# Kernel optimization log

Measured on AMD Instinct MI355X. Metric: run time of the kernel, lower is better.

The kernel has to match this reference:

```python
import jax, jax.numpy as jnp
import numpy as np
import math

D_MODEL = 512
D_HEAD = 64
N_HEADS = D_MODEL // D_HEAD  # 8
COND = 768
K = 7        # neighborhood kernel size
EPS = 1e-6


def _rope_freqs():
    # RoPE(dim=d_head//2, n_heads): freqs geometric in [pi, 10*pi), shape [n_heads, d_head//4]
    dim = D_HEAD // 2
    n = N_HEADS * dim // 2
    freqs = jnp.exp(jnp.linspace(math.log(math.pi), math.log(10.0 * math.pi), n + 1)[:-1])
    return freqs.reshape(dim // 2, N_HEADS).T  # [nh, d_head//4]


def _rms_norm(x, scale, eps):
    mean_sq = jnp.mean(x * x, axis=-1, keepdims=True)
    return x * (scale * jax.lax.rsqrt(mean_sq + eps))


def _apply_rotary(x, theta):
    # rotate first 2*d dims of head dim, leave the rest untouched
    d = theta.shape[-1]
    x1, x2, rest = x[..., :d], x[..., d:2 * d], x[..., 2 * d:]
    cos, sin = jnp.cos(theta), jnp.sin(theta)
    return jnp.concatenate([x1 * cos - x2 * sin, x2 * cos + x1 * sin, rest], axis=-1)


def _nb_idx(L, k):
    # NATTEN border handling: window shifts (clamps) so every query sees exactly k keys
    i = np.arange(L)
    start = np.clip(i - k // 2, 0, L - k)
    return jnp.asarray(start[:, None] + np.arange(k)[None, :])  # [L, k]


def setup_inputs() -> dict:
    key = jax.random.key(0)
    ks = jax.random.split(key, 7)
    N, H, W = 2, 32, 32
    x = jax.random.normal(ks[0], (N, H, W, D_MODEL), jnp.float32)
    pos = jax.random.uniform(ks[1], (N, H, W, 1), jnp.float32, -1.0, 1.0)
    cond = jax.random.normal(ks[2], (N, COND), jnp.float32)
    w_cond = jax.random.normal(ks[3], (D_MODEL, COND), jnp.float32) * 0.02
    w_qkv = jax.random.normal(ks[4], (3 * D_MODEL, D_MODEL), jnp.float32) * 0.02
    scale = jnp.full((N_HEADS,), 10.0, jnp.float32)
    w_out = jax.random.normal(ks[5], (D_MODEL, D_MODEL), jnp.float32) * 0.02
    return {"x": x, "pos": pos, "cond": cond, "w_cond": w_cond,
            "w_qkv": w_qkv, "scale": scale, "w_out": w_out}


def reference(x, pos, cond, w_cond, w_qkv, scale, w_out):
    N, H, W, C = x.shape
    skip = x
    # AdaRMSNorm: rms_norm(x, linear(cond) + 1)
    norm_scale = cond @ w_cond.T + 1.0                  # [N, C]
    xn = _rms_norm(x, norm_scale[:, None, None, :], EPS)
    # qkv projection -> [3, N, nh, H, W, e]
    qkv = (xn @ w_qkv.T).reshape(N, H, W, 3, N_HEADS, D_HEAD)
    qkv = qkv.transpose(3, 0, 4, 1, 2, 5)
    q, k, v = qkv[0], qkv[1], qkv[2]                    # [N, nh, H, W, e]
    # cosine-sim scaling
    sq = jnp.sqrt(scale)[:, None, None, None]           # [nh,1,1,1]
    q = q * (sq * jax.lax.rsqrt(jnp.sum(q * q, -1, keepdims=True) + 1e-6))
    k = k * (sq * jax.lax.rsqrt(jnp.sum(k * k, -1, keepdims=True) + 1e-6))
    # RoPE
    theta = pos[..., None, :] * _rope_freqs()           # [N,H,W,nh,e/4]
    theta = jnp.moveaxis(theta, -2, -4)                 # [N,nh,H,W,e/4]
    q = _apply_rotary(q, theta)
    k = _apply_rotary(k, theta)
    # 2D neighborhood attention (NATTEN, dilation 1)
    ih, iw = _nb_idx(H, K), _nb_idx(W, K)
    Knb = k[:, :, ih][:, :, :, :, iw]                   # [N,nh,H,K,W,K,e]
    Vnb = v[:, :, ih][:, :, :, :, iw]
    qk = jnp.einsum('ncije,nciajbe->ncijab', q, Knb)    # [N,nh,H,W,K,K]
    a = jax.nn.softmax(qk.reshape(N, N_HEADS, H, W, K * K), axis=-1)
    a = a.reshape(N, N_HEADS, H, W, K, K)
    o = jnp.einsum('ncijab,nciajbe->ncije', a, Vnb)     # [N,nh,H,W,e]
    o = o.transpose(0, 2, 3, 1, 4).reshape(N, H, W, C)
    return o @ w_out.T + skip
```

## Files before the change

kernel.cpp:

```cpp
#include <hip/hip_runtime.h>

typedef unsigned short u16;
typedef unsigned int u32;
typedef __bf16 bf16x8 __attribute__((ext_vector_type(8)));
typedef float f32x4 __attribute__((ext_vector_type(4)));

__device__ __forceinline__ float bf2f(u16 v) {
    union { u32 u; float f; } c; c.u = ((u32)v) << 16; return c.f;
}
__device__ __forceinline__ u16 f2bf(float f) {
    union { float f; u32 u; } c; c.f = f;
    u32 u = c.u + 0x7fffu + ((c.u >> 16) & 1u);
    return (u16)(u >> 16);
}

__global__ __launch_bounds__(256) void cond_kernel(
    const float* __restrict__ cond, const float* __restrict__ w_cond, float* __restrict__ ns)
{
    int lane = threadIdx.x & 63;
    int wid = blockIdx.x * 4 + (threadIdx.x >> 6);
    int n = wid >> 9, c = wid & 511;
    const float* cp = cond + n * 768;
    const float* wp = w_cond + (size_t)c * 768;
    float s = 0.f;
    #pragma unroll
    for (int j = 0; j < 12; j++)
        s += cp[lane + j * 64] * wp[lane + j * 64];
    #pragma unroll
    for (int d = 1; d < 64; d <<= 1) s += __shfl_xor(s, d);
    if (lane == 0) ns[wid] = s + 1.f;
}

__global__ __launch_bounds__(256) void prep_kernel(
    const float* __restrict__ x, const float* __restrict__ ns,
    const float* __restrict__ w_qkv, const float* __restrict__ w_out,
    u16* __restrict__ xn, u16* __restrict__ wqkvb, u16* __restrict__ woutb)
{
    int b = blockIdx.x;
    if (b < 512) {
        int w = threadIdx.x >> 6, lane = threadIdx.x & 63;
        int p = b * 4 + w;
        int n = p >> 10;
        const float* xp = x + (size_t)p * 512;
        const float* nsp = ns + n * 512;
        float4 v0 = *(const float4*)(xp + lane * 4);
        float4 v1 = *(const float4*)(xp + 256 + lane * 4);
        float ss = v0.x * v0.x + v0.y * v0.y + v0.z * v0.z + v0.w * v0.w
                 + v1.x * v1.x + v1.y * v1.y + v1.z * v1.z + v1.w * v1.w;
        #pragma unroll
        for (int d = 1; d < 64; d <<= 1) ss += __shfl_xor(ss, d);
        float inv = rsqrtf(ss * (1.f / 512.f) + 1e-6f);
        float4 n0 = *(const float4*)(nsp + lane * 4);
        float4 n1 = *(const float4*)(nsp + 256 + lane * 4);
        ushort4 o0, o1;
        o0.x = f2bf(v0.x * n0.x * inv); o0.y = f2bf(v0.y * n0.y * inv);
        o0.z = f2bf(v0.z * n0.z * inv); o0.w = f2bf(v0.w * n0.w * inv);
        o1.x = f2bf(v1.x * n1.x * inv); o1.y = f2bf(v1.y * n1.y * inv);
        o1.z = f2bf(v1.z * n1.z * inv); o1.w = f2bf(v1.w * n1.w * inv);
        *(ushort4*)(xn + (size_t)p * 512 + lane * 4) = o0;
        *(ushort4*)(xn + (size_t)p * 512 + 256 + lane * 4) = o1;
    } else {
        const float* src; u16* dst; size_t i4;
        if (b < 1280) { src = w_qkv; dst = wqkvb; i4 = (size_t)(b - 512)  * 1024 + threadIdx.x * 4; }
        else          { src = w_out; dst = woutb; i4 = (size_t)(b - 1280) * 1024 + threadIdx.x * 4; }
        float4 v = *(const float4*)(src + i4);
        ushort4 o; o.x = f2bf(v.x); o.y = f2bf(v.y); o.z = f2bf(v.z); o.w = f2bf(v.w);
        *(ushort4*)(dst + i4) = o;
    }
}

__global__ __launch_bounds__(256) void gemm_qkv(
    const u16* __restrict__ A, const u16* __restrict__ B,
    const float* __restrict__ pos, const float* __restrict__ scale,
    u16* __restrict__ qp, u16* __restrict__ kp, u16* __restrict__ vp)
{
    __shared__ __align__(16) u16 As[4][64][40];
    __shared__ __align__(16) u16 Bs[4][64][40];
    int tid = threadIdx.x;
    int lane = tid & 63;
    int w = tid >> 6;
    int wm = w >> 1, wn = w & 1;
    int bm = blockIdx.x * 64, bn = blockIdx.y * 64;
    int qk = blockIdx.y >> 3, h = blockIdx.y & 7;
    int lrow = tid >> 2, lc8 = (tid & 3) * 8;

    f32x4 zero = {0.f, 0.f, 0.f, 0.f};
    f32x4 acc[2][2];
    acc[0][0] = zero; acc[0][1] = zero; acc[1][0] = zero; acc[1][1] = zero;

    const u16* Ap = A + (size_t)(bm + lrow) * 512 + lc8;
    const u16* Bp = B + (size_t)(bn + lrow) * 512 + lc8;
    int m = lane & 15, quad = lane >> 4, kq = quad * 8;

    for (int k0 = 0; k0 < 512; k0 += 128) {
        #pragma unroll
        for (int s = 0; s < 4; s++) {
            *(uint4*)&As[s][lrow][lc8] = *(const uint4*)(Ap + k0 + s * 32);
            *(uint4*)&Bs[s][lrow][lc8] = *(const uint4*)(Bp + k0 + s * 32);
        }
        __syncthreads();
        #pragma unroll
        for (int kk = 0; kk < 4; kk++)
        #pragma unroll
        for (int ri = 0; ri < 2; ri++) {
            bf16x8 af = *(const bf16x8*)&As[kk][wm * 32 + ri * 16 + m][kq];
            #pragma unroll
            for (int ci = 0; ci < 2; ci++) {
                bf16x8 bfr = *(const bf16x8*)&Bs[kk][wn * 32 + ci * 16 + m][kq];
                acc[ri][ci] = __builtin_amdgcn_mfma_f32_16x16x32_bf16(af, bfr, acc[ri][ci], 0, 0, 0);
            }
        }
        __syncthreads();
    }

    float invn[2][4];
    if (qk < 2) {
        float* red = (float*)As;
        #pragma unroll
        for (int ri = 0; ri < 2; ri++)
        #pragma unroll
        for (int reg = 0; reg < 4; reg++) {
            float pa = acc[ri][0][reg] * acc[ri][0][reg]
                     + acc[ri][1][reg] * acc[ri][1][reg];
            #pragma unroll
            for (int d = 1; d < 16; d <<= 1) pa += __shfl_xor(pa, d);
            if (m == 0) red[(wm * 32 + ri * 16 + quad * 4 + reg) * 2 + wn] = pa;
        }
        __syncthreads();
        float sq = sqrtf(scale[h]);
        #pragma unroll
        for (int ri = 0; ri < 2; ri++)
        #pragma unroll
        for (int reg = 0; reg < 4; reg++) {
            int rl = wm * 32 + ri * 16 + quad * 4 + reg;
            invn[ri][reg] = sq * rsqrtf(red[rl * 2] + red[rl * 2 + 1] + 1e-6f);
        }
    }
    u16* plane = (qk == 0) ? qp : (qk == 1) ? kp : vp;
    float fr = 3.14159265358979323846f * expf((float)(m * 8 + h) * (2.302585092994046f / 128.f));
    #pragma unroll
    for (int ri = 0; ri < 2; ri++)
    #pragma unroll
    for (int reg = 0; reg < 4; reg++) {
        int rl = wm * 32 + ri * 16 + quad * 4 + reg;
        int p = bm + rl;
        size_t basep = ((size_t)((p >> 10) * 8 + h) * 1024 + (p & 1023)) * 64;
        float v0 = acc[ri][0][reg], v1 = acc[ri][1][reg];
        if (qk < 2) {
            float ivn = invn[ri][reg];
            v0 *= ivn; v1 *= ivn;
            if (wn == 0) {
                float th = pos[p] * fr;
                float cs = cosf(th), sn = sinf(th);
                float o0 = v0 * cs - v1 * sn;
                float o1 = v1 * cs + v0 * sn;
                v0 = o0; v1 = o1;
            }
        }
        plane[basep + wn * 32 + m]      = f2bf(v0);
        plane[basep + wn * 32 + 16 + m] = f2bf(v1);
    }
}

__global__ __launch_bounds__(256) void gemm_out(
    const u16* __restrict__ A, const u16* __restrict__ B,
    float* __restrict__ C, const float* __restrict__ skip, int N, int K)
{
    __shared__ __align__(16) u16 As[4][64][40];
    __shared__ __align__(16) u16 Bs[4][64][40];
    int tid = threadIdx.x;
    int lane = tid & 63;
    int w = tid >> 6;
    int wm = w >> 1, wn = w & 1;
    int bm = blockIdx.x * 64, bn = blockIdx.y * 64;
    int lrow = tid >> 2, lc8 = (tid & 3) * 8;

    f32x4 zero = {0.f, 0.f, 0.f, 0.f};
    f32x4 acc[2][2];
    acc[0][0] = zero; acc[0][1] = zero; acc[1][0] = zero; acc[1][1] = zero;

    const u16* Ap = A + (size_t)(bm + lrow) * K + lc8;
    const u16* Bp = B + (size_t)(bn + lrow) * K + lc8;
    int r = lane & 15, kq = (lane >> 4) * 8;

    for (int k0 = 0; k0 < K; k0 += 128) {
        #pragma unroll
        for (int s = 0; s < 4; s++) {
            *(uint4*)&As[s][lrow][lc8] = *(const uint4*)(Ap + k0 + s * 32);
            *(uint4*)&Bs[s][lrow][lc8] = *(const uint4*)(Bp + k0 + s * 32);
        }
        __syncthreads();
        #pragma unroll
        for (int kk = 0; kk < 4; kk++)
        #pragma unroll
        for (int ri = 0; ri < 2; ri++) {
            bf16x8 af = *(const bf16x8*)&As[kk][wm * 32 + ri * 16 + r][kq];
            #pragma unroll
            for (int ci = 0; ci < 2; ci++) {
                bf16x8 bfr = *(const bf16x8*)&Bs[kk][wn * 32 + ci * 16 + r][kq];
                acc[ri][ci] = __builtin_amdgcn_mfma_f32_16x16x32_bf16(af, bfr, acc[ri][ci], 0, 0, 0);
            }
        }
        __syncthreads();
    }

    #pragma unroll
    for (int ri = 0; ri < 2; ri++)
    #pragma unroll
    for (int ci = 0; ci < 2; ci++) {
        int col = bn + wn * 32 + ci * 16 + (lane & 15);
        int row0 = bm + wm * 32 + ri * 16 + (lane >> 4) * 4;
        #pragma unroll
        for (int reg = 0; reg < 4; reg++) {
            size_t idx = (size_t)(row0 + reg) * N + col;
            C[idx] = acc[ri][ci][reg] + skip[idx];
        }
    }
}

__global__ __launch_bounds__(256) void attn_mfma(
    const u16* __restrict__ qp, const u16* __restrict__ kp, const u16* __restrict__ vp,
    u16* __restrict__ ob)
{
    __shared__ __align__(16) u16 Kb[208 * 72];
    __shared__ __align__(16) u16 Sb[64 * 232];

    int tid = threadIdx.x, lane = tid & 63, w = tid >> 6;
    int bx = blockIdx.x;
    int n = bx >> 7, h = (bx >> 4) & 7, t = bx & 15;
    int ti = (t >> 2) * 8, tj = (t & 3) * 8;
    int r0 = min(max(ti - 3, 0), 18), c0 = min(max(tj - 3, 0), 18);
    const u16* qpl = qp + ((size_t)(n * 8 + h) << 16);
    const u16* kpl = kp + ((size_t)(n * 8 + h) << 16);
    const u16* vpl = vp + ((size_t)(n * 8 + h) << 16);

    for (int g = tid; g < 1568; g += 256) {
        int nb = g >> 3, k8 = (g & 7) << 3;
        int ar = nb / 14, ac = nb - ar * 14;
        *(uint4*)&Kb[nb * 72 + k8] =
            *(const uint4*)&kpl[(size_t)((r0 + ar) * 32 + c0 + ac) * 64 + k8];
    }
    __syncthreads();

    int m = lane & 15, quad = lane >> 4;
    {
        int r = w * 16 + m;
        int tok = (ti + (r >> 3)) * 32 + (tj + (r & 7));
        bf16x8 qf0 = *(const bf16x8*)&qpl[(size_t)tok * 64 + quad * 8];
        bf16x8 qf1 = *(const bf16x8*)&qpl[(size_t)tok * 64 + 32 + quad * 8];
        _Float16* sp = (_Float16*)Sb;
        #pragma unroll
        for (int nt = 0; nt < 13; nt++) {
            f32x4 acc = {0.f, 0.f, 0.f, 0.f};
            bf16x8 b0 = *(const bf16x8*)&Kb[(nt * 16 + m) * 72 + quad * 8];
            bf16x8 b1 = *(const bf16x8*)&Kb[(nt * 16 + m) * 72 + 32 + quad * 8];
            acc = __builtin_amdgcn_mfma_f32_16x16x32_bf16(qf0, b0, acc, 0, 0, 0);
            acc = __builtin_amdgcn_mfma_f32_16x16x32_bf16(qf1, b1, acc, 0, 0, 0);
            #pragma unroll
            for (int reg = 0; reg < 4; reg++)
                sp[(w * 16 + quad * 4 + reg) * 232 + nt * 16 + m] = (_Float16)acc[reg];
        }
    }
    __syncthreads();

    for (int g = tid; g < 1568; g += 256) {
        int nb = g >> 3, k8 = (g & 7) << 3;
        int ar = nb / 14, ac = nb - ar * 14;
        uint4 v4 = *(const uint4*)&vpl[(size_t)((r0 + ar) * 32 + c0 + ac) * 64 + k8];
        u32 uu[4] = {v4.x, v4.y, v4.z, v4.w};
        #pragma unroll
        for (int e = 0; e < 4; e++) {
            Kb[(k8 + 2 * e) * 234 + nb]     = (u16)(uu[e] & 0xffff);
            Kb[(k8 + 2 * e + 1) * 234 + nb] = (u16)(uu[e] >> 16);
        }
    }
    for (int g = tid; g < 1792; g += 256) {
        int d = g / 28, nb = 196 + (g - d * 28);
        Kb[d * 234 + nb] = 0;
    }

    {
        int l16 = lane & 15, g4 = lane >> 4;
        #pragma unroll
        for (int it = 0; it < 4; it++) {
            int rr = w * 16 + it * 4 + g4;
            int i2 = ti + (rr >> 3), j2 = tj + (rr & 7);
            int alo = min(max(i2 - 3, 0), 25) - r0;
            int blo = min(max(j2 - 3, 0), 25) - c0;
            const _Float16* sp = (const _Float16*)&Sb[rr * 232];
            float vals[14];
            float mx = -1e30f;
            #pragma unroll
            for (int c = 0; c < 14; c++) {
                int col = l16 + c * 16;
                float v = -1e30f;
                if (col < 196) {
                    int ar = col / 14, ac = col - ar * 14;
                    if (ar >= alo && ar < alo + 7 && ac >= blo && ac < blo + 7)
                        v = (float)sp[col];
                }
                vals[c] = v; mx = fmaxf(mx, v);
            }
            #pragma unroll
            for (int d = 1; d < 16; d <<= 1) mx = fmaxf(mx, __shfl_xor(mx, d));
            float s = 0.f;
            #pragma unroll
            for (int c = 0; c < 14; c++) {
                float e = (vals[c] > -1e29f) ? expf(vals[c] - mx) : 0.f;
                vals[c] = e; s += e;
            }
            #pragma unroll
            for (int d = 1; d < 16; d <<= 1) s += __shfl_xor(s, d);
            float rs = __frcp_rn(s);
            u16* pp = &Sb[rr * 232];
            #pragma unroll
            for (int c = 0; c < 14; c++)
                pp[l16 + c * 16] = f2bf(vals[c] * rs);
        }
    }
    __syncthreads();

    f32x4 oacc[4];
    #pragma unroll
    for (int nt = 0; nt < 4; nt++) { f32x4 z = {0.f,0.f,0.f,0.f}; oacc[nt] = z; }
    #pragma unroll
    for (int ks = 0; ks < 7; ks++) {
        bf16x8 pa = *(const bf16x8*)&Sb[(w * 16 + m) * 232 + ks * 32 + quad * 8];
        #pragma unroll
        for (int nt = 0; nt < 4; nt++) {
            int ad = (nt * 16 + m) * 234 + ks * 32 + quad * 8;
            union { u32 u[4]; bf16x8 v; } vb;
            vb.u[0] = *(const u32*)&Kb[ad];
            vb.u[1] = *(const u32*)&Kb[ad + 2];
            vb.u[2] = *(const u32*)&Kb[ad + 4];
            vb.u[3] = *(const u32*)&Kb[ad + 6];
            oacc[nt] = __builtin_amdgcn_mfma_f32_16x16x32_bf16(pa, vb.v, oacc[nt], 0, 0, 0);
        }
    }
    #pragma unroll
    for (int nt = 0; nt < 4; nt++) {
        #pragma unroll
        for (int reg = 0; reg < 4; reg++) {
            int rr = w * 16 + quad * 4 + reg;
            int tok = (ti + (rr >> 3)) * 32 + (tj + (rr & 7));
            ob[(size_t)(n * 1024 + tok) * 512 + h * 64 + nt * 16 + m] = f2bf(oacc[nt][reg]);
        }
    }
}

extern "C" void kernel_launch(void* const* d_in, const int* in_sizes, int n_in,
                              void* d_out, int out_size, void* d_ws, size_t ws_size,
                              hipStream_t stream)
{
    const float *x = nullptr, *pos = nullptr, *cond = nullptr, *w_cond = nullptr,
                *w_qkv = nullptr, *scale = nullptr, *w_out = nullptr;
    for (int i = 0; i < n_in; i++) {
        switch (in_sizes[i]) {
            case 1048576: x      = (const float*)d_in[i]; break;
            case 2048:    pos    = (const float*)d_in[i]; break;
            case 1536:    cond   = (const float*)d_in[i]; break;
            case 393216:  w_cond = (const float*)d_in[i]; break;
            case 786432:  w_qkv  = (const float*)d_in[i]; break;
            case 8:       scale  = (const float*)d_in[i]; break;
            case 262144:  w_out  = (const float*)d_in[i]; break;
            default: break;
        }
    }
    float* out = (float*)d_out;

    char* ws = (char*)d_ws;
    float* ns    = (float*)ws;
    u16*   wqkvb = (u16*)(ws + 12288);
    u16*   woutb = (u16*)(ws + 12288 + 1572864);
    u16*   xn    = (u16*)(ws + 12288 + 2097152);
    u16*   qp    = (u16*)(ws + 12288 + 4194304);
    u16*   kp    = (u16*)(ws + 12288 + 6291456);
    u16*   vp    = (u16*)(ws + 12288 + 8388608);
    u16*   ob    = (u16*)(ws + 12288 + 10485760);

    cond_kernel<<<256, 256, 0, stream>>>(cond, w_cond, ns);
    prep_kernel<<<1536, 256, 0, stream>>>(x, ns, w_qkv, w_out, xn, wqkvb, woutb);
    gemm_qkv<<<dim3(32, 24), 256, 0, stream>>>(xn, wqkvb, pos, scale, qp, kp, vp);
    attn_mfma<<<256, 256, 0, stream>>>(qp, kp, vp, ob);
    gemm_out<<<dim3(32, 8), 256, 0, stream>>>(ob, woutb, out, x, 512, 512);
}
```

Before: 109.9 us.

## Rebalance prep kernels, double attention block threads, hoist MFMA fragment loads

Moves the weight bf16 conversion into the cond kernel and gives RMS-norm its own launch, so the cond matvec and the weight casts share one grid. The attention kernel now runs 512 threads per block: QK tiles, softmax rows and PV output columns are split across 8 waves, and s_setprio is raised around the MFMAs. The exp mask check is replaced with exp2f. Both GEMM inner loops load their A/B fragments once per k-step before issuing four MFMAs. More waves per attention block mean more parallelism over the same LDS buffers, but also more barrier cost and an uneven 7/6 split of the 13 QK tiles.

```diff
diff --git a/kernel.cpp b/kernel.cpp
--- a/kernel.cpp
+++ b/kernel.cpp
@@ -14,59 +14,60 @@
     return (u16)(u >> 16);
 }
 
-__global__ __launch_bounds__(256) void cond_kernel(
-    const float* __restrict__ cond, const float* __restrict__ w_cond, float* __restrict__ ns)
-{
-    int lane = threadIdx.x & 63;
-    int wid = blockIdx.x * 4 + (threadIdx.x >> 6);
-    int n = wid >> 9, c = wid & 511;
-    const float* cp = cond + n * 768;
-    const float* wp = w_cond + (size_t)c * 768;
-    float s = 0.f;
-    #pragma unroll
-    for (int j = 0; j < 12; j++)
-        s += cp[lane + j * 64] * wp[lane + j * 64];
-    #pragma unroll
-    for (int d = 1; d < 64; d <<= 1) s += __shfl_xor(s, d);
-    if (lane == 0) ns[wid] = s + 1.f;
-}
-
-__global__ __launch_bounds__(256) void prep_kernel(
-    const float* __restrict__ x, const float* __restrict__ ns,
+__global__ __launch_bounds__(256) void cond_prepw_kernel(
+    const float* __restrict__ cond, const float* __restrict__ w_cond, float* __restrict__ ns,
     const float* __restrict__ w_qkv, const float* __restrict__ w_out,
-    u16* __restrict__ xn, u16* __restrict__ wqkvb, u16* __restrict__ woutb)
+    u16* __restrict__ wqkvb, u16* __restrict__ woutb)
 {
     int b = blockIdx.x;
-    if (b < 512) {
-        int w = threadIdx.x >> 6, lane = threadIdx.x & 63;
-        int p = b * 4 + w;
-        int n = p >> 10;
-        const float* xp = x + (size_t)p * 512;
-        const float* nsp = ns + n * 512;
-        float4 v0 = *(const float4*)(xp + lane * 4);
-        float4 v1 = *(const float4*)(xp + 256 + lane * 4);
-        float ss = v0.x * v0.x + v0.y * v0.y + v0.z * v0.z + v0.w * v0.w
-                 + v1.x * v1.x + v1.y * v1.y + v1.z * v1.z + v1.w * v1.w;
-        #pragma unroll
-        for (int d = 1; d < 64; d <<= 1) ss += __shfl_xor(ss, d);
-        float inv = rsqrtf(ss * (1.f / 512.f) + 1e-6f);
-        float4 n0 = *(const float4*)(nsp + lane * 4);
-        float4 n1 = *(const float4*)(nsp + 256 + lane * 4);
-        ushort4 o0, o1;
-        o0.x = f2bf(v0.x * n0.x * inv); o0.y = f2bf(v0.y * n0.y * inv);
-        o0.z = f2bf(v0.z * n0.z * inv); o0.w = f2bf(v0.w * n0.w * inv);
-        o1.x = f2bf(v1.x * n1.x * inv); o1.y = f2bf(v1.y * n1.y * inv);
-        o1.z = f2bf(v1.z * n1.z * inv); o1.w = f2bf(v1.w * n1.w * inv);
-        *(ushort4*)(xn + (size_t)p * 512 + lane * 4) = o0;
-        *(ushort4*)(xn + (size_t)p * 512 + 256 + lane * 4) = o1;
+    if (b < 256) {
+        int lane = threadIdx.x & 63;
+        int wid = b * 4 + (threadIdx.x >> 6);
+        int n = wid >> 9, c = wid & 511;
+        const float* cp = cond + n * 768;
+        const float* wp = w_cond + (size_t)c * 768;
+        float s = 0.f;
+        #pragma unroll
+        for (int j = 0; j < 12; j++)
+            s += cp[lane + j * 64] * wp[lane + j * 64];
+        #pragma unroll
+        for (int d = 1; d < 64; d <<= 1) s += __shfl_xor(s, d);
+        if (lane == 0) ns[wid] = s + 1.f;
     } else {
         const float* src; u16* dst; size_t i4;
-        if (b < 1280) { src = w_qkv; dst = wqkvb; i4 = (size_t)(b - 512)  * 1024 + threadIdx.x * 4; }
-        else          { src = w_out; dst = woutb; i4 = (size_t)(b - 1280) * 1024 + threadIdx.x * 4; }
+        if (b < 1024) { src = w_qkv; dst = wqkvb; i4 = (size_t)(b - 256)  * 1024 + threadIdx.x * 4; }
+        else          { src = w_out; dst = woutb; i4 = (size_t)(b - 1024) * 1024 + threadIdx.x * 4; }
         float4 v = *(const float4*)(src + i4);
         ushort4 o; o.x = f2bf(v.x); o.y = f2bf(v.y); o.z = f2bf(v.z); o.w = f2bf(v.w);
         *(ushort4*)(dst + i4) = o;
     }
+}
+
+__global__ __launch_bounds__(256) void rms_kernel(
+    const float* __restrict__ x, const float* __restrict__ ns, u16* __restrict__ xn)
+{
+    int b = blockIdx.x;
+    int w = threadIdx.x >> 6, lane = threadIdx.x & 63;
+    int p = b * 4 + w;
+    int n = p >> 10;
+    const float* xp = x + (size_t)p * 512;
+    const float* nsp = ns + n * 512;
+    float4 v0 = *(const float4*)(xp + lane * 4);
+    float4 v1 = *(const float4*)(xp + 256 + lane * 4);
+    float ss = v0.x * v0.x + v0.y * v0.y + v0.z * v0.z + v0.w * v0.w
+             + v1.x * v1.x + v1.y * v1.y + v1.z * v1.z + v1.w * v1.w;
+    #pragma unroll
+    for (int d = 1; d < 64; d <<= 1) ss += __shfl_xor(ss, d);
+    float inv = rsqrtf(ss * (1.f / 512.f) + 1e-6f);
+    float4 n0 = *(const float4*)(nsp + lane * 4);
+    float4 n1 = *(const float4*)(nsp + 256 + lane * 4);
+    ushort4 o0, o1;
+    o0.x = f2bf(v0.x * n0.x * inv); o0.y = f2bf(v0.y * n0.y * inv);
+    o0.z = f2bf(v0.z * n0.z * inv); o0.w = f2bf(v0.w * n0.w * inv);
+    o1.x = f2bf(v1.x * n1.x * inv); o1.y = f2bf(v1.y * n1.y * inv);
+    o1.z = f2bf(v1.z * n1.z * inv); o1.w = f2bf(v1.w * n1.w * inv);
+    *(ushort4*)(xn + (size_t)p * 512 + lane * 4) = o0;
+    *(ushort4*)(xn + (size_t)p * 512 + 256 + lane * 4) = o1;
 }
 
 __global__ __launch_bounds__(256) void gemm_qkv(
@@ -100,15 +101,15 @@
         }
         __syncthreads();
         #pragma unroll
-        for (int kk = 0; kk < 4; kk++)
-        #pragma unroll
-        for (int ri = 0; ri < 2; ri++) {
-            bf16x8 af = *(const bf16x8*)&As[kk][wm * 32 + ri * 16 + m][kq];
-            #pragma unroll
-            for (int ci = 0; ci < 2; ci++) {
-                bf16x8 bfr = *(const bf16x8*)&Bs[kk][wn * 32 + ci * 16 + m][kq];
-                acc[ri][ci] = __builtin_amdgcn_mfma_f32_16x16x32_bf16(af, bfr, acc[ri][ci], 0, 0, 0);
-            }
+        for (int kk = 0; kk < 4; kk++) {
+            bf16x8 a0 = *(const bf16x8*)&As[kk][wm * 32 + m][kq];
+            bf16x8 a1 = *(const bf16x8*)&As[kk][wm * 32 + 16 + m][kq];
+            bf16x8 b0 = *(const bf16x8*)&Bs[kk][wn * 32 + m][kq];
+            bf16x8 b1 = *(const bf16x8*)&Bs[kk][wn * 32 + 16 + m][kq];
+            acc[0][0] = __builtin_amdgcn_mfma_f32_16x16x32_bf16(a0, b0, acc[0][0], 0, 0, 0);
+            acc[0][1] = __builtin_amdgcn_mfma_f32_16x16x32_bf16(a0, b1, acc[0][1], 0, 0, 0);
+            acc[1][0] = __builtin_amdgcn_mfma_f32_16x16x32_bf16(a1, b0, acc[1][0], 0, 0, 0);
+            acc[1][1] = __builtin_amdgcn_mfma_f32_16x16x32_bf16(a1, b1, acc[1][1], 0, 0, 0);
         }
         __syncthreads();
     }
@@ -191,15 +192,15 @@
         }
         __syncthreads();
         #pragma unroll
-        for (int kk = 0; kk < 4; kk++)
-        #pragma unroll
-        for (int ri = 0; ri < 2; ri++) {
-            bf16x8 af = *(const bf16x8*)&As[kk][wm * 32 + ri * 16 + r][kq];
-            #pragma unroll
-            for (int ci = 0; ci < 2; ci++) {
-                bf16x8 bfr = *(const bf16x8*)&Bs[kk][wn * 32 + ci * 16 + r][kq];
-                acc[ri][ci] = __builtin_amdgcn_mfma_f32_16x16x32_bf16(af, bfr, acc[ri][ci], 0, 0, 0);
-            }
+        for (int kk = 0; kk < 4; kk++) {
+            bf16x8 a0 = *(const bf16x8*)&As[kk][wm * 32 + r][kq];
+            bf16x8 a1 = *(const bf16x8*)&As[kk][wm * 32 + 16 + r][kq];
+            bf16x8 b0 = *(const bf16x8*)&Bs[kk][wn * 32 + r][kq];
+            bf16x8 b1 = *(const bf16x8*)&Bs[kk][wn * 32 + 16 + r][kq];
+            acc[0][0] = __builtin_amdgcn_mfma_f32_16x16x32_bf16(a0, b0, acc[0][0], 0, 0, 0);
+            acc[0][1] = __builtin_amdgcn_mfma_f32_16x16x32_bf16(a0, b1, acc[0][1], 0, 0, 0);
+            acc[1][0] = __builtin_amdgcn_mfma_f32_16x16x32_bf16(a1, b0, acc[1][0], 0, 0, 0);
+            acc[1][1] = __builtin_amdgcn_mfma_f32_16x16x32_bf16(a1, b1, acc[1][1], 0, 0, 0);
         }
         __syncthreads();
     }
@@ -218,7 +219,7 @@
     }
 }
 
-__global__ __launch_bounds__(256) void attn_mfma(
+__global__ __launch_bounds__(512) void attn_mfma(
     const u16* __restrict__ qp, const u16* __restrict__ kp, const u16* __restrict__ vp,
     u16* __restrict__ ob)
 {
@@ -234,7 +235,7 @@
     const u16* kpl = kp + ((size_t)(n * 8 + h) << 16);
     const u16* vpl = vp + ((size_t)(n * 8 + h) << 16);
 
-    for (int g = tid; g < 1568; g += 256) {
+    for (int g = tid; g < 1568; g += 512) {
         int nb = g >> 3, k8 = (g & 7) << 3;
         int ar = nb / 14, ac = nb - ar * 14;
         *(uint4*)&Kb[nb * 72 + k8] =
@@ -243,27 +244,32 @@
     __syncthreads();
 
     int m = lane & 15, quad = lane >> 4;
+    int rg = w & 3, half = w >> 2;
     {
-        int r = w * 16 + m;
+        int r = rg * 16 + m;
         int tok = (ti + (r >> 3)) * 32 + (tj + (r & 7));
         bf16x8 qf0 = *(const bf16x8*)&qpl[(size_t)tok * 64 + quad * 8];
         bf16x8 qf1 = *(const bf16x8*)&qpl[(size_t)tok * 64 + 32 + quad * 8];
         _Float16* sp = (_Float16*)Sb;
-        #pragma unroll
-        for (int nt = 0; nt < 13; nt++) {
+        int ntb = half * 7;
+        int ntn = 7 - half;
+        for (int i = 0; i < ntn; i++) {
+            int nt = ntb + i;
             f32x4 acc = {0.f, 0.f, 0.f, 0.f};
             bf16x8 b0 = *(const bf16x8*)&Kb[(nt * 16 + m) * 72 + quad * 8];
             bf16x8 b1 = *(const bf16x8*)&Kb[(nt * 16 + m) * 72 + 32 + quad * 8];
+            __builtin_amdgcn_s_setprio(1);
             acc = __builtin_amdgcn_mfma_f32_16x16x32_bf16(qf0, b0, acc, 0, 0, 0);
             acc = __builtin_amdgcn_mfma_f32_16x16x32_bf16(qf1, b1, acc, 0, 0, 0);
+            __builtin_amdgcn_s_setprio(0);
             #pragma unroll
             for (int reg = 0; reg < 4; reg++)
-                sp[(w * 16 + quad * 4 + reg) * 232 + nt * 16 + m] = (_Float16)acc[reg];
+                sp[(rg * 16 + quad * 4 + reg) * 232 + nt * 16 + m] = (_Float16)acc[reg];
         }
     }
     __syncthreads();
 
-    for (int g = tid; g < 1568; g += 256) {
+    for (int g = tid; g < 1568; g += 512) {
         int nb = g >> 3, k8 = (g & 7) << 3;
         int ar = nb / 14, ac = nb - ar * 14;
         uint4 v4 = *(const uint4*)&vpl[(size_t)((r0 + ar) * 32 + c0 + ac) * 64 + k8];
@@ -274,7 +280,7 @@
             Kb[(k8 + 2 * e + 1) * 234 + nb] = (u16)(uu[e] >> 16);
         }
     }
-    for (int g = tid; g < 1792; g += 256) {
+    for (int g = tid; g < 1792; g += 512) {
         int d = g / 28, nb = 196 + (g - d * 28);
         Kb[d * 234 + nb] = 0;
     }
@@ -282,8 +288,8 @@
     {
         int l16 = lane & 15, g4 = lane >> 4;
         #pragma unroll
-        for (int it = 0; it < 4; it++) {
-            int rr = w * 16 + it * 4 + g4;
+        for (int it = 0; it < 2; it++) {
+            int rr = w * 8 + it * 4 + g4;
             int i2 = ti + (rr >> 3), j2 = tj + (rr & 7);
             int alo = min(max(i2 - 3, 0), 25) - r0;
             int blo = min(max(j2 - 3, 0), 25) - c0;
@@ -306,7 +312,7 @@
             float s = 0.f;
             #pragma unroll
             for (int c = 0; c < 14; c++) {
-                float e = (vals[c] > -1e29f) ? expf(vals[c] - mx) : 0.f;
+                float e = exp2f((vals[c] - mx) * 1.44269504f);
                 vals[c] = e; s += e;
             }
             #pragma unroll
@@ -320,30 +326,36 @@
     }
     __syncthreads();
 
-    f32x4 oacc[4];
-    #pragma unroll
-    for (int nt = 0; nt < 4; nt++) { f32x4 z = {0.f,0.f,0.f,0.f}; oacc[nt] = z; }
+    f32x4 oacc[2];
+    {
+        f32x4 z = {0.f, 0.f, 0.f, 0.f};
+        oacc[0] = z; oacc[1] = z;
+    }
     #pragma unroll
     for (int ks = 0; ks < 7; ks++) {
-        bf16x8 pa = *(const bf16x8*)&Sb[(w * 16 + m) * 232 + ks * 32 + quad * 8];
-        #pragma unroll
-        for (int nt = 0; nt < 4; nt++) {
+        bf16x8 pa = *(const bf16x8*)&Sb[(rg * 16 + m) * 232 + ks * 32 + quad * 8];
+        __builtin_amdgcn_s_setprio(1);
+        #pragma unroll
+        for (int j = 0; j < 2; j++) {
+            int nt = half * 2 + j;
             int ad = (nt * 16 + m) * 234 + ks * 32 + quad * 8;
             union { u32 u[4]; bf16x8 v; } vb;
             vb.u[0] = *(const u32*)&Kb[ad];
             vb.u[1] = *(const u32*)&Kb[ad + 2];
             vb.u[2] = *(const u32*)&Kb[ad + 4];
             vb.u[3] = *(const u32*)&Kb[ad + 6];
-            oacc[nt] = __builtin_amdgcn_mfma_f32_16x16x32_bf16(pa, vb.v, oacc[nt], 0, 0, 0);
-        }
-    }
-    #pragma unroll
-    for (int nt = 0; nt < 4; nt++) {
+            oacc[j] = __builtin_amdgcn_mfma_f32_16x16x32_bf16(pa, vb.v, oacc[j], 0, 0, 0);
+        }
+        __builtin_amdgcn_s_setprio(0);
+    }
+    #pragma unroll
+    for (int j = 0; j < 2; j++) {
+        int nt = half * 2 + j;
         #pragma unroll
         for (int reg = 0; reg < 4; reg++) {
-            int rr = w * 16 + quad * 4 + reg;
+            int rr = rg * 16 + quad * 4 + reg;
             int tok = (ti + (rr >> 3)) * 32 + (tj + (rr & 7));
-            ob[(size_t)(n * 1024 + tok) * 512 + h * 64 + nt * 16 + m] = f2bf(oacc[nt][reg]);
+            ob[(size_t)(n * 1024 + tok) * 512 + h * 64 + nt * 16 + m] = f2bf(oacc[j][reg]);
         }
     }
 }
@@ -378,9 +390,9 @@
     u16*   vp    = (u16*)(ws + 12288 + 8388608);
     u16*   ob    = (u16*)(ws + 12288 + 10485760);
 
-    cond_kernel<<<256, 256, 0, stream>>>(cond, w_cond, ns);
-    prep_kernel<<<1536, 256, 0, stream>>>(x, ns, w_qkv, w_out, xn, wqkvb, woutb);
+    cond_prepw_kernel<<<1280, 256, 0, stream>>>(cond, w_cond, ns, w_qkv, w_out, wqkvb, woutb);
+    rms_kernel<<<512, 256, 0, stream>>>(x, ns, xn);
     gemm_qkv<<<dim3(32, 24), 256, 0, stream>>>(xn, wqkvb, pos, scale, qp, kp, vp);
-    attn_mfma<<<256, 256, 0, stream>>>(qp, kp, vp, ob);
+    attn_mfma<<<256, 512, 0, stream>>>(qp, kp, vp, ob);
     gemm_out<<<dim3(32, 8), 256, 0, stream>>>(ob, woutb, out, x, 512, 512);
 }
```

After: 105.2 us. 4.3% less time.
